# Kernel tuning notes

Measured on AMD Instinct MI355X. Metric: run time of the kernel, lower is better.

## Reference

```python
import jax, jax.numpy as jnp
import numpy as np
from jax import lax

B, T, F, H, NC = 64, 256, 64, 128, 2


def setup_inputs() -> dict:
    key = jax.random.key(0)
    ks = jax.random.split(key, 10)
    # timestamps: sorted ints with duplicates -> exercises per-timestamp mean aggregation
    t = jnp.sort(jax.random.randint(ks[0], (B, T), 0, T // 2), axis=1).astype(jnp.float32)
    m = jax.random.randint(ks[1], (B, T), 0, F).astype(jnp.float32)
    x = jax.random.normal(ks[2], (B, T), dtype=jnp.float32)
    delt = jax.random.uniform(ks[3], (B, T), dtype=jnp.float32)
    X = jnp.stack([t, m, x, delt], axis=1)  # [B, 4, T]
    lengths = jax.random.randint(ks[4], (B,), T // 2, T + 1).astype(jnp.int32)
    s = 1.0 / np.sqrt(H + 1)
    W_lin = jax.random.uniform(ks[5], (F, H + 1, 4 * H), minval=-s, maxval=s, dtype=jnp.float32)
    b_lin = jax.random.uniform(ks[6], (F, 4 * H), minval=-s, maxval=s, dtype=jnp.float32)
    W_dec = jax.random.uniform(ks[7], (F,), minval=-1.0, maxval=1.0, dtype=jnp.float32)
    b_dec = jax.random.uniform(ks[8], (F,), minval=-1.0, maxval=1.0, dtype=jnp.float32)
    so = 1.0 / np.sqrt(F * H + H)
    k9, k10 = jax.random.split(ks[9])
    W_out = jax.random.uniform(k9, (F * H + H, NC), minval=-so, maxval=so, dtype=jnp.float32)
    b_out = jax.random.uniform(k10, (NC,), minval=-so, maxval=so, dtype=jnp.float32)
    return {"X": X, "lengths": lengths, "W_lin": W_lin, "b_lin": b_lin,
            "W_dec": W_dec, "b_dec": b_dec, "W_out": W_out, "b_out": b_out}


def _forward(X, lengths, W_lin, b_lin, W_dec, b_dec, W_out, b_out):
    nF, Hp1, H4 = W_lin.shape
    hs = Hp1 - 1
    t = X[:, 0]
    m = X[:, 1].astype(jnp.int32)
    x = X[:, 2]
    delt = X[:, 3]
    idx = jnp.arange(t.shape[1])
    valid = idx[None, :] < lengths[:, None]                       # event is real
    t_next = jnp.concatenate([t[:, 1:], t[:, -1:] + 1.0], axis=1)
    # last event of a consecutive-equal-timestamp group (within valid length)
    boundary = (idx[None, :] == (lengths[:, None] - 1)) | (t_next != t)

    def per_sample(m_s, x_s, d_s, v_s, b_s):
        def step(carry, inp):
            h_t, c_t, acc, cnt = carry
            mj, xj, dj, vj, bj = inp
            # feature-specific decay of that feature's hidden row
            dm = W_dec[mj] * dj + b_dec[mj]
            decay = jnp.exp(-jnp.maximum(0.0, dm))
            h_dec = decay * h_t[mj]
            inp_vec = jnp.concatenate([xj[None], h_dec])          # [H+1]
            gates = inp_vec @ W_lin[mj] + b_lin[mj]               # [4H]
            gi, gf, go, gc = jnp.split(gates, 4)
            c_cand = jax.nn.sigmoid(gf) * c_t + jax.nn.sigmoid(gi) * jnp.tanh(gc)
            h_row = jax.nn.sigmoid(go) * jnp.tanh(c_cand)
            h_t = jnp.where(vj, h_t.at[mj].set(h_row), h_t)
            acc = acc + jnp.where(vj, c_cand, 0.0)
            cnt = cnt + jnp.where(vj, 1.0, 0.0)
            close = vj & bj                                       # end of timestamp group
            c_t = jnp.where(close, acc / jnp.maximum(cnt, 1.0), c_t)
            acc = jnp.where(close, jnp.zeros_like(acc), acc)
            cnt = jnp.where(close, 0.0, cnt)
            return (h_t, c_t, acc, cnt), None

        init = (jnp.zeros((nF, hs), jnp.float32), jnp.zeros((hs,), jnp.float32),
                jnp.zeros((hs,), jnp.float32), jnp.float32(0.0))
        (h_t, c_t, _, _), _ = lax.scan(step, init, (m_s, x_s, d_s, v_s, b_s))
        feats = jnp.concatenate([c_t, h_t.reshape(-1)])           # [H + F*H]
        return jax.nn.softmax(feats @ W_out + b_out)

    return jax.vmap(per_sample)(m, x, delt, valid, boundary)      # [B, n_class]


def reference(X, lengths, W_lin, b_lin, W_dec, b_dec, W_out, b_out):
    return _forward(X, lengths, W_lin, b_lin, W_dec, b_dec, W_out, b_out)
```

## Files before the change

kernel.cpp:

```cpp
#include <hip/hip_runtime.h>
#include <math.h>

#define BATCH 64
#define T 256
#define NF 64
#define H 128
#define H4 512
#define HP1 129
#define WF_STRIDE (HP1 * H4)
#define FEATS (NF * H + H)
#define NTHREADS 512
#define PACK_UINT4_PER_F 8192
#define PACK_BYTES (64u * PACK_UINT4_PER_F * 16u)

typedef _Float16 half2_t __attribute__((ext_vector_type(2)));

__device__ __forceinline__ float sigmoidf_(float x) {
    return 1.0f / (1.0f + __expf(-x));
}

__device__ __forceinline__ float tanhf_(float x) {
    float ax = fabsf(x);
    float e = __expf(2.0f * ax);
    float r = 1.0f - 2.0f / (e + 1.0f);
    return copysignf(r, x);
}

__device__ __forceinline__ float fdot2_(half2_t a, half2_t b, float c) {
#if defined(__has_builtin)
#if __has_builtin(__builtin_amdgcn_fdot2)
    return __builtin_amdgcn_fdot2(a, b, c, false);
#else
    return fmaf((float)a.x, (float)b.x, fmaf((float)a.y, (float)b.y, c));
#endif
#else
    return fmaf((float)a.x, (float)b.x, fmaf((float)a.y, (float)b.y, c));
#endif
}

__global__ __launch_bounds__(256)
void repack_kernel(const float* __restrict__ W_lin, uint4* __restrict__ pack) {
    const int lin = blockIdx.x * 256 + threadIdx.x;
    const int f   = lin >> 13;
    const int i   = (lin >> 9) & 15;
    const int tid = lin & 511;
    const int kq  = tid >> 7;
    const int g4  = tid & 127;
    const int k0  = kq * 32 + 2 * i;
    const float* src = W_lin + (size_t)f * WF_STRIDE + (size_t)(1 + k0) * H4 + 4 * g4;
    const float4 r0 = *(const float4*)(src);
    const float4 r1 = *(const float4*)(src + H4);
    half2_t h[4];
    h[0].x = (_Float16)r0.x; h[0].y = (_Float16)r1.x;
    h[1].x = (_Float16)r0.y; h[1].y = (_Float16)r1.y;
    h[2].x = (_Float16)r0.z; h[2].y = (_Float16)r1.z;
    h[3].x = (_Float16)r0.w; h[3].y = (_Float16)r1.w;
    pack[lin] = *(uint4*)h;
}

__global__ __launch_bounds__(NTHREADS, 2)
void lstm_scan_fp16_kernel(const float* __restrict__ X,
                           const int* __restrict__ lengths,
                           const float* __restrict__ W_lin,
                           const float* __restrict__ b_lin,
                           const float* __restrict__ W_dec,
                           const float* __restrict__ b_dec,
                           const float* __restrict__ W_out,
                           const float* __restrict__ b_out,
                           const uint4* __restrict__ pack,
                           float* __restrict__ out)
{
    __shared__ float s_feats[FEATS];
    __shared__ half2_t s_inp2[H / 2];
    __shared__ float s_part[4][H4];
    __shared__ float s_X[4 * T];
    __shared__ float s_wdec[NF];
    __shared__ float s_bdec[NF];
    __shared__ float s_red[16];

    float* s_ct = s_feats;
    float* s_ht = s_feats + H;

    const int tid = threadIdx.x;
    const int b   = blockIdx.x;
    const int g4  = tid & 127;
    const int kq  = tid >> 7;

    const float* Xb = X + b * 4 * T;
    const int len = lengths[b];

    for (int i = tid; i < NF * H; i += NTHREADS) s_ht[i] = 0.0f;
    for (int i = tid; i < 4 * T; i += NTHREADS) s_X[i] = Xb[i];
    if (tid < NF) { s_wdec[tid] = W_dec[tid]; s_bdec[tid] = b_dec[tid]; }
    if (tid < H / 2) { half2_t z; z.x = (_Float16)0.0f; z.y = (_Float16)0.0f; s_inp2[tid] = z; }
    __syncthreads();

    float c_t = 0.0f, acc = 0.0f, cnt = 0.0f;

    uint4 bufA[16], bufB[16];
    {
        const int m0 = (int)s_X[T];
        const uint4* Wp = pack + m0 * PACK_UINT4_PER_F + tid;
        #pragma unroll
        for (int i = 0; i < 16; ++i) bufA[i] = Wp[i * 512];
    }

    #define STEP(CUR, NXT)                                                          \
    {                                                                               \
        const int   mj = (int)s_X[T + j];                                           \
        const float xj = s_X[2 * T + j];                                            \
        const int   jn = (j + 1 < T) ? (j + 1) : (T - 1);                           \
        const int   mjn = (int)s_X[T + jn];                                         \
                                                  \
        {                                                                           \
            const uint4* Wp = pack + mjn * PACK_UINT4_PER_F + tid;                  \
            _Pragma("unroll")                                                       \
            for (int i = 0; i < 16; ++i) NXT[i] = Wp[i * 512];                      \
        }                                                                           \
                       \
        float bl0, bl1, bl2, bl3;                                                   \
        if (tid < H) {                                                              \
            const int m4 = mj * H4;                                                 \
            bl0 = b_lin[m4 + tid];                                                  \
            bl1 = b_lin[m4 + H + tid];                                              \
            bl2 = b_lin[m4 + 2 * H + tid];                                          \
            bl3 = b_lin[m4 + 3 * H + tid];                                          \
        }                                                                           \
                                               \
        float a0 = 0.0f, a1 = 0.0f, a2 = 0.0f, a3 = 0.0f;                           \
        _Pragma("unroll")                                                           \
        for (int i = 0; i < 16; ++i) {                                              \
            union { uint4 u; half2_t h[4]; } cv;                                    \
            cv.u = CUR[i];                                                          \
            const half2_t iv = s_inp2[kq * 16 + i];                                 \
            a0 = fdot2_(cv.h[0], iv, a0);                                           \
            a1 = fdot2_(cv.h[1], iv, a1);                                           \
            a2 = fdot2_(cv.h[2], iv, a2);                                           \
            a3 = fdot2_(cv.h[3], iv, a3);                                           \
        }                                                                           \
        if (kq == 0) {                         \
            const float4 w = *(const float4*)(W_lin + (size_t)mj * WF_STRIDE + 4 * g4); \
            a0 = fmaf(xj, w.x, a0); a1 = fmaf(xj, w.y, a1);                         \
            a2 = fmaf(xj, w.z, a2); a3 = fmaf(xj, w.w, a3);                         \
        }                                                                           \
        float4 a4; a4.x = a0; a4.y = a1; a4.z = a2; a4.w = a3;                      \
        *(float4*)(&s_part[kq][4 * g4]) = a4;                                       \
        __syncthreads();                                     \
        if (tid < H) {                                                              \
            const int h = tid;                                                      \
            const float gi = s_part[0][h]         + s_part[1][h]         + s_part[2][h]         + s_part[3][h]         + bl0; \
            const float gf = s_part[0][H + h]     + s_part[1][H + h]     + s_part[2][H + h]     + s_part[3][H + h]     + bl1; \
            const float go = s_part[0][2*H + h]   + s_part[1][2*H + h]   + s_part[2][2*H + h]   + s_part[3][2*H + h]   + bl2; \
            const float gc = s_part[0][3*H + h]   + s_part[1][3*H + h]   + s_part[2][3*H + h]   + s_part[3][3*H + h]   + bl3; \
            const float c_cand = sigmoidf_(gf) * c_t + sigmoidf_(gi) * tanhf_(gc);  \
            const float h_row  = sigmoidf_(go) * tanhf_(c_cand);                    \
            s_ht[mj * H + h] = h_row;                                               \
            acc += c_cand;                                                          \
            cnt += 1.0f;                                                            \
            const float tj = s_X[j];                                                \
            const float tn = (j < T - 1) ? s_X[j + 1] : (tj + 1.0f);                \
            const bool boundary = (j == len - 1) || (tn != tj);                     \
            if (boundary) { c_t = acc / fmaxf(cnt, 1.0f); acc = 0.0f; cnt = 0.0f; } \
                                      \
            const float dn  = s_X[3 * T + jn];                                      \
            const float dmn = fmaf(s_wdec[mjn], dn, s_bdec[mjn]);                   \
            const float den = __expf(-fmaxf(0.0f, dmn));                            \
            const float hv  = (mjn == mj) ? h_row : s_ht[mjn * H + h];              \
            ((_Float16*)s_inp2)[h] = (_Float16)(den * hv);                          \
        }                                                                           \
        __syncthreads();                                 \
    }

    int j = 0;
    while (j < len) {
        STEP(bufA, bufB); ++j;
        if (j >= len) break;
        STEP(bufB, bufA); ++j;
    }
    #undef STEP

    if (tid < H) s_ct[tid] = c_t;
    __syncthreads();

    float z0 = 0.0f, z1 = 0.0f;
    for (int i = tid; i < FEATS; i += NTHREADS) {
        const float f = s_feats[i];
        const float2 w = *(const float2*)(W_out + 2 * i);
        z0 = fmaf(f, w.x, z0);
        z1 = fmaf(f, w.y, z1);
    }
    #pragma unroll
    for (int off = 32; off > 0; off >>= 1) {
        z0 += __shfl_down(z0, off, 64);
        z1 += __shfl_down(z1, off, 64);
    }
    const int wave = tid >> 6, lane = tid & 63;
    if (lane == 0) { s_red[2 * wave] = z0; s_red[2 * wave + 1] = z1; }
    __syncthreads();
    if (tid == 0) {
        float a0 = b_out[0], a1 = b_out[1];
        #pragma unroll
        for (int w = 0; w < 8; ++w) { a0 += s_red[2 * w]; a1 += s_red[2 * w + 1]; }
        const float mx = fmaxf(a0, a1);
        const float e0 = __expf(a0 - mx), e1 = __expf(a1 - mx);
        const float inv = 1.0f / (e0 + e1);
        out[2 * b]     = e0 * inv;
        out[2 * b + 1] = e1 * inv;
    }
}

__global__ __launch_bounds__(NTHREADS)
void lstm_scan_kernel(const float* __restrict__ X,
                      const int* __restrict__ lengths,
                      const float* __restrict__ W_lin,
                      const float* __restrict__ b_lin,
                      const float* __restrict__ W_dec,
                      const float* __restrict__ b_dec,
                      const float* __restrict__ W_out,
                      const float* __restrict__ b_out,
                      float* __restrict__ out)
{
    __shared__ float s_feats[FEATS];
    __shared__ float s_inp[H];
    __shared__ float s_part[4][H4];
    __shared__ float s_X[4 * T];
    __shared__ float s_wdec[NF];
    __shared__ float s_bdec[NF];
    __shared__ float s_red[16];

    float* s_ct = s_feats;
    float* s_ht = s_feats + H;

    const int tid = threadIdx.x;
    const int b   = blockIdx.x;
    const int g4  = tid & 127;
    const int kq  = tid >> 7;

    const float* Xb = X + b * 4 * T;
    const int len = lengths[b];

    for (int i = tid; i < NF * H; i += NTHREADS) s_ht[i] = 0.0f;
    for (int i = tid; i < 4 * T; i += NTHREADS) s_X[i] = Xb[i];
    if (tid < NF) { s_wdec[tid] = W_dec[tid]; s_bdec[tid] = b_dec[tid]; }
    __syncthreads();

    float c_t = 0.0f, acc = 0.0f, cnt = 0.0f;

    for (int j = 0; j < len; ++j) {
        const int   mj = (int)s_X[T + j];
        const float xj = s_X[2 * T + j];
        const float* Wf = W_lin + mj * WF_STRIDE;

        float bl0, bl1, bl2, bl3;
        if (tid < H) {
            const float dj    = s_X[3 * T + j];
            const float dm    = fmaf(s_wdec[mj], dj, s_bdec[mj]);
            const float decay = __expf(-fmaxf(0.0f, dm));
            s_inp[tid] = decay * s_ht[mj * H + tid];
            const int m4 = mj * H4;
            bl0 = b_lin[m4 + tid];
            bl1 = b_lin[m4 + H + tid];
            bl2 = b_lin[m4 + 2 * H + tid];
            bl3 = b_lin[m4 + 3 * H + tid];
        }
        __syncthreads();

        float4 a4 = make_float4(0.0f, 0.0f, 0.0f, 0.0f);
        {
            const float*  wr  = Wf + (1 + kq * 32) * H4 + 4 * g4;
            const float4* ivp = (const float4*)(s_inp + kq * 32);
            #pragma unroll
            for (int c = 0; c < 8; ++c) {
                const float4 v = ivp[c];
                const float* wrc = wr + (4 * c) * H4;
                const float4 w0 = *(const float4*)(wrc);
                const float4 w1 = *(const float4*)(wrc + H4);
                const float4 w2 = *(const float4*)(wrc + 2 * H4);
                const float4 w3 = *(const float4*)(wrc + 3 * H4);
                a4.x = fmaf(v.x, w0.x, a4.x); a4.y = fmaf(v.x, w0.y, a4.y);
                a4.z = fmaf(v.x, w0.z, a4.z); a4.w = fmaf(v.x, w0.w, a4.w);
                a4.x = fmaf(v.y, w1.x, a4.x); a4.y = fmaf(v.y, w1.y, a4.y);
                a4.z = fmaf(v.y, w1.z, a4.z); a4.w = fmaf(v.y, w1.w, a4.w);
                a4.x = fmaf(v.z, w2.x, a4.x); a4.y = fmaf(v.z, w2.y, a4.y);
                a4.z = fmaf(v.z, w2.z, a4.z); a4.w = fmaf(v.z, w2.w, a4.w);
                a4.x = fmaf(v.w, w3.x, a4.x); a4.y = fmaf(v.w, w3.y, a4.y);
                a4.z = fmaf(v.w, w3.z, a4.z); a4.w = fmaf(v.w, w3.w, a4.w);
            }
        }
        if (kq == 0) {
            const float4 w = *(const float4*)(Wf + 4 * g4);
            a4.x = fmaf(xj, w.x, a4.x); a4.y = fmaf(xj, w.y, a4.y);
            a4.z = fmaf(xj, w.z, a4.z); a4.w = fmaf(xj, w.w, a4.w);
        }
        *(float4*)(&s_part[kq][4 * g4]) = a4;
        __syncthreads();

        if (tid < H) {
            const int h = tid;
            const float gi = s_part[0][h]         + s_part[1][h]         + s_part[2][h]         + s_part[3][h]         + bl0;
            const float gf = s_part[0][H + h]     + s_part[1][H + h]     + s_part[2][H + h]     + s_part[3][H + h]     + bl1;
            const float go = s_part[0][2*H + h]   + s_part[1][2*H + h]   + s_part[2][2*H + h]   + s_part[3][2*H + h]   + bl2;
            const float gc = s_part[0][3*H + h]   + s_part[1][3*H + h]   + s_part[2][3*H + h]   + s_part[3][3*H + h]   + bl3;

            const float c_cand = sigmoidf_(gf) * c_t + sigmoidf_(gi) * tanhf_(gc);
            const float h_row  = sigmoidf_(go) * tanhf_(c_cand);
            s_ht[mj * H + h] = h_row;
            acc += c_cand;
            cnt += 1.0f;

            const float tj = s_X[j];
            const float tn = (j < T - 1) ? s_X[j + 1] : (tj + 1.0f);
            const bool boundary = (j == len - 1) || (tn != tj);
            if (boundary) { c_t = acc / fmaxf(cnt, 1.0f); acc = 0.0f; cnt = 0.0f; }
        }
        __syncthreads();
    }

    if (tid < H) s_ct[tid] = c_t;
    __syncthreads();

    float z0 = 0.0f, z1 = 0.0f;
    for (int i = tid; i < FEATS; i += NTHREADS) {
        const float f = s_feats[i];
        const float2 w = *(const float2*)(W_out + 2 * i);
        z0 = fmaf(f, w.x, z0);
        z1 = fmaf(f, w.y, z1);
    }
    #pragma unroll
    for (int off = 32; off > 0; off >>= 1) {
        z0 += __shfl_down(z0, off, 64);
        z1 += __shfl_down(z1, off, 64);
    }
    const int wave = tid >> 6, lane = tid & 63;
    if (lane == 0) { s_red[2 * wave] = z0; s_red[2 * wave + 1] = z1; }
    __syncthreads();
    if (tid == 0) {
        float a0 = b_out[0], a1 = b_out[1];
        #pragma unroll
        for (int w = 0; w < 8; ++w) { a0 += s_red[2 * w]; a1 += s_red[2 * w + 1]; }
        const float mx = fmaxf(a0, a1);
        const float e0 = __expf(a0 - mx), e1 = __expf(a1 - mx);
        const float inv = 1.0f / (e0 + e1);
        out[2 * b]     = e0 * inv;
        out[2 * b + 1] = e1 * inv;
    }
}

extern "C" void kernel_launch(void* const* d_in, const int* in_sizes, int n_in,
                              void* d_out, int out_size, void* d_ws, size_t ws_size,
                              hipStream_t stream) {
    const float* X      = (const float*)d_in[0];
    const int*   lens   = (const int*)d_in[1];
    const float* W_lin  = (const float*)d_in[2];
    const float* b_lin  = (const float*)d_in[3];
    const float* W_dec  = (const float*)d_in[4];
    const float* b_dec  = (const float*)d_in[5];
    const float* W_out  = (const float*)d_in[6];
    const float* b_out  = (const float*)d_in[7];
    float* out = (float*)d_out;

    if (ws_size >= (size_t)PACK_BYTES) {
        uint4* pack = (uint4*)d_ws;
        hipLaunchKernelGGL(repack_kernel, dim3(2048), dim3(256), 0, stream, W_lin, pack);
        hipLaunchKernelGGL(lstm_scan_fp16_kernel, dim3(BATCH), dim3(NTHREADS), 0, stream,
                           X, lens, W_lin, b_lin, W_dec, b_dec, W_out, b_out, pack, out);
    } else {
        hipLaunchKernelGGL(lstm_scan_kernel, dim3(BATCH), dim3(NTHREADS), 0, stream,
                           X, lens, W_lin, b_lin, W_dec, b_dec, W_out, b_out, out);
    }
}
```

Measured before the change: 526.7 us.

## Prefetch weights two steps ahead and spread gate nonlinearities across all threads

The kernel now preloads two timesteps of packed fp16 weights and refills each buffer right after it is consumed, so weight fetches have about two steps of latency to hide. The bias and x-weight loads for the next step are issued before the barrier and carried in registers. Gate activations are now computed by all 512 threads through a new shared s_gate array, replacing the 128-thread serial sigmoid and tanh work, and the input vector is read with vectorized shared loads. This adds one extra __syncthreads per step and increases register pressure.

```diff
diff --git a/kernel.cpp b/kernel.cpp
--- a/kernel.cpp
+++ b/kernel.cpp
@@ -71,8 +71,9 @@
                            float* __restrict__ out)
 {
     __shared__ float s_feats[FEATS];
-    __shared__ half2_t s_inp2[H / 2];
+    __shared__ __align__(16) half2_t s_inp2[H / 2];
     __shared__ float s_part[4][H4];
+    __shared__ float s_gate[H4];
     __shared__ float s_X[4 * T];
     __shared__ float s_wdec[NF];
     __shared__ float s_bdec[NF];
@@ -98,84 +99,108 @@
     float c_t = 0.0f, acc = 0.0f, cnt = 0.0f;
 
     uint4 bufA[16], bufB[16];
+    float b_cur;
+    float4 wx;
+    float xj_cur;
     {
-        const int m0 = (int)s_X[T];
-        const uint4* Wp = pack + m0 * PACK_UINT4_PER_F + tid;
+        const int m0 = (int)Xb[T];
+        const int m1v = (int)Xb[T + 1];
+        const uint4* Wp0 = pack + m0 * PACK_UINT4_PER_F + tid;
+        const uint4* Wp1 = pack + m1v * PACK_UINT4_PER_F + tid;
         #pragma unroll
-        for (int i = 0; i < 16; ++i) bufA[i] = Wp[i * 512];
-    }
-
-    #define STEP(CUR, NXT)                                                          \
+        for (int i = 0; i < 16; ++i) bufA[i] = Wp0[i * 512];
+        #pragma unroll
+        for (int i = 0; i < 16; ++i) bufB[i] = Wp1[i * 512];
+        b_cur = b_lin[m0 * H4 + tid];
+        if (kq == 0) wx = *(const float4*)(W_lin + (size_t)m0 * WF_STRIDE + 4 * g4);
+        xj_cur = Xb[2 * T];
+    }
+
+    #define STEP(CUR)                                                               \
     {                                                                               \
-        const int   mj = (int)s_X[T + j];                                           \
-        const float xj = s_X[2 * T + j];                                            \
-        const int   jn = (j + 1 < T) ? (j + 1) : (T - 1);                           \
-        const int   mjn = (int)s_X[T + jn];                                         \
-                                                  \
+        const int mj = (int)s_X[T + j];                                             \
+                              \
+        half2_t iv[16];                                                             \
         {                                                                           \
-            const uint4* Wp = pack + mjn * PACK_UINT4_PER_F + tid;                  \
-            _Pragma("unroll")                                                       \
-            for (int i = 0; i < 16; ++i) NXT[i] = Wp[i * 512];                      \
-        }                                                                           \
-                       \
-        float bl0, bl1, bl2, bl3;                                                   \
-        if (tid < H) {                                                              \
-            const int m4 = mj * H4;                                                 \
-            bl0 = b_lin[m4 + tid];                                                  \
-            bl1 = b_lin[m4 + H + tid];                                              \
-            bl2 = b_lin[m4 + 2 * H + tid];                                          \
-            bl3 = b_lin[m4 + 3 * H + tid];                                          \
-        }                                                                           \
-                                               \
+            const uint4* ivp = (const uint4*)s_inp2;                                \
+            *(uint4*)(&iv[0])  = ivp[kq * 4 + 0];                                   \
+            *(uint4*)(&iv[4])  = ivp[kq * 4 + 1];                                   \
+            *(uint4*)(&iv[8])  = ivp[kq * 4 + 2];                                   \
+            *(uint4*)(&iv[12]) = ivp[kq * 4 + 3];                                   \
+        }                                                                           \
         float a0 = 0.0f, a1 = 0.0f, a2 = 0.0f, a3 = 0.0f;                           \
         _Pragma("unroll")                                                           \
         for (int i = 0; i < 16; ++i) {                                              \
             union { uint4 u; half2_t h[4]; } cv;                                    \
             cv.u = CUR[i];                                                          \
-            const half2_t iv = s_inp2[kq * 16 + i];                                 \
-            a0 = fdot2_(cv.h[0], iv, a0);                                           \
-            a1 = fdot2_(cv.h[1], iv, a1);                                           \
-            a2 = fdot2_(cv.h[2], iv, a2);                                           \
-            a3 = fdot2_(cv.h[3], iv, a3);                                           \
-        }                                                                           \
-        if (kq == 0) {                         \
-            const float4 w = *(const float4*)(W_lin + (size_t)mj * WF_STRIDE + 4 * g4); \
-            a0 = fmaf(xj, w.x, a0); a1 = fmaf(xj, w.y, a1);                         \
-            a2 = fmaf(xj, w.z, a2); a3 = fmaf(xj, w.w, a3);                         \
-        }                                                                           \
-        float4 a4; a4.x = a0; a4.y = a1; a4.z = a2; a4.w = a3;                      \
-        *(float4*)(&s_part[kq][4 * g4]) = a4;                                       \
+            a0 = fdot2_(cv.h[0], iv[i], a0);                                        \
+            a1 = fdot2_(cv.h[1], iv[i], a1);                                        \
+            a2 = fdot2_(cv.h[2], iv[i], a2);                                        \
+            a3 = fdot2_(cv.h[3], iv[i], a3);                                        \
+        }                                                                           \
+        if (kq == 0) {               \
+            a0 = fmaf(xj_cur, wx.x, a0); a1 = fmaf(xj_cur, wx.y, a1);               \
+            a2 = fmaf(xj_cur, wx.z, a2); a3 = fmaf(xj_cur, wx.w, a3);               \
+        }                                                                           \
+        { float4 a4; a4.x = a0; a4.y = a1; a4.z = a2; a4.w = a3;                    \
+          *(float4*)(&s_part[kq][4 * g4]) = a4; }                                   \
+               \
+        {                                                                           \
+            const int j2 = (j + 2 < T) ? (j + 2) : (T - 1);                         \
+            const int m2 = (int)s_X[T + j2];                                        \
+            const uint4* Wp = pack + m2 * PACK_UINT4_PER_F + tid;                   \
+            _Pragma("unroll")                                                       \
+            for (int i = 0; i < 16; ++i) CUR[i] = Wp[i * 512];                      \
+        }                                                                           \
+                                     \
+        const int   j1 = (j + 1 < T) ? (j + 1) : (T - 1);                           \
+        const int   m1 = (int)s_X[T + j1];                                          \
+        const float b_nx = b_lin[m1 * H4 + tid];                                    \
+        float4 wx_nx;                                                               \
+        if (kq == 0) wx_nx = *(const float4*)(W_lin + (size_t)m1 * WF_STRIDE + 4 * g4); \
+        const float xj_nx = s_X[2 * T + j1];                                        \
         __syncthreads();                                     \
+              \
+        {                                                                           \
+            const float gsum = s_part[0][tid] + s_part[1][tid]                      \
+                             + s_part[2][tid] + s_part[3][tid] + b_cur;             \
+            s_gate[tid] = (tid >= 3 * H) ? tanhf_(gsum) : sigmoidf_(gsum);          \
+        }                                                                           \
+        __syncthreads();                                        \
         if (tid < H) {                                                              \
             const int h = tid;                                                      \
-            const float gi = s_part[0][h]         + s_part[1][h]         + s_part[2][h]         + s_part[3][h]         + bl0; \
-            const float gf = s_part[0][H + h]     + s_part[1][H + h]     + s_part[2][H + h]     + s_part[3][H + h]     + bl1; \
-            const float go = s_part[0][2*H + h]   + s_part[1][2*H + h]   + s_part[2][2*H + h]   + s_part[3][2*H + h]   + bl2; \
-            const float gc = s_part[0][3*H + h]   + s_part[1][3*H + h]   + s_part[2][3*H + h]   + s_part[3][3*H + h]   + bl3; \
-            const float c_cand = sigmoidf_(gf) * c_t + sigmoidf_(gi) * tanhf_(gc);  \
-            const float h_row  = sigmoidf_(go) * tanhf_(c_cand);                    \
+            const float nl_i = s_gate[h];                                           \
+            const float nl_f = s_gate[H + h];                                       \
+            const float nl_o = s_gate[2 * H + h];                                   \
+            const float nl_c = s_gate[3 * H + h];                                   \
+            const float c_cand = nl_f * c_t + nl_i * nl_c;                          \
+            const float h_row  = nl_o * tanhf_(c_cand);                             \
             s_ht[mj * H + h] = h_row;                                               \
             acc += c_cand;                                                          \
             cnt += 1.0f;                                                            \
             const float tj = s_X[j];                                                \
             const float tn = (j < T - 1) ? s_X[j + 1] : (tj + 1.0f);                \
-            const bool boundary = (j == len - 1) || (tn != tj);                     \
-            if (boundary) { c_t = acc / fmaxf(cnt, 1.0f); acc = 0.0f; cnt = 0.0f; } \
+            if ((j == len - 1) || (tn != tj)) {                                     \
+                c_t = acc / fmaxf(cnt, 1.0f); acc = 0.0f; cnt = 0.0f;               \
+            }                                                                       \
                                       \
-            const float dn  = s_X[3 * T + jn];                                      \
-            const float dmn = fmaf(s_wdec[mjn], dn, s_bdec[mjn]);                   \
+            const float dn  = s_X[3 * T + j1];                                      \
+            const float dmn = fmaf(s_wdec[m1], dn, s_bdec[m1]);                     \
             const float den = __expf(-fmaxf(0.0f, dmn));                            \
-            const float hv  = (mjn == mj) ? h_row : s_ht[mjn * H + h];              \
+            const float hv  = (m1 == mj) ? h_row : s_ht[m1 * H + h];                \
             ((_Float16*)s_inp2)[h] = (_Float16)(den * hv);                          \
         }                                                                           \
         __syncthreads();                                 \
+        b_cur = b_nx;                                                               \
+        if (kq == 0) wx = wx_nx;                                                    \
+        xj_cur = xj_nx;                                                             \
     }
 
     int j = 0;
     while (j < len) {
-        STEP(bufA, bufB); ++j;
+        STEP(bufA); ++j;
         if (j >= len) break;
-        STEP(bufB, bufA); ++j;
+        STEP(bufB); ++j;
     }
     #undef STEP
 
```

Measured after the change: 527.4 us. No clear change (+0.1%).
